# Kernel tuning notes

Hardware: AMD Instinct MI355X
Metric: run time of the kernel (lower is better)

The kernel has to match this reference:

```python
import jax, jax.numpy as jnp
import numpy as np


def setup_inputs() -> dict:
    key = jax.random.key(0)
    ks = jax.random.split(key, 6)
    N, n, m = 8, 256, 256
    d_q, d_k, d_v, hidden = 256, 256, 256, 256
    scale_q = 1.0 / np.sqrt(d_q)
    scale_k = 1.0 / np.sqrt(d_k)
    scale_h = 1.0 / np.sqrt(hidden)
    return {
        "query": jax.random.normal(ks[0], (N, n, d_q), dtype=jnp.float32),
        "key": jax.random.normal(ks[1], (N, m, d_k), dtype=jnp.float32),
        "value": jax.random.normal(ks[2], (N, m, d_v), dtype=jnp.float32),
        # Linear weights stored as (in, out) so projection is x @ W
        "Wq": jax.random.normal(ks[3], (d_q, hidden), dtype=jnp.float32) * scale_q,
        "Wk": jax.random.normal(ks[4], (d_k, hidden), dtype=jnp.float32) * scale_k,
        "Wv": jax.random.normal(ks[5], (hidden,), dtype=jnp.float32) * scale_h,
        "choose": 0,
    }


def reference(query, key, value, Wq, Wk, Wv, choose):
    if choose == 0:
        q = jnp.einsum('bnd,dh->bnh', query, Wq)   # (N, n, h)
        k = jnp.einsum('bmd,dh->bmh', key, Wk)     # (N, m, h)
        # broadcast-add + tanh, then contract hidden with W_v -> scores (N, n, m)
        features = jnp.tanh(q[:, :, None, :] + k[:, None, :, :])  # (N, n, m, h)
        scores = jnp.einsum('bnmh,h->bnm', features, Wv)
        # NOTE: original applies softmax over dim=1 (query axis) — preserved
        attn_weights = jax.nn.softmax(scores, axis=1)
    else:
        d = query.shape[2]
        scores = jnp.einsum('bnd,bmd->bnm', query, key) / jnp.sqrt(jnp.float32(d))
        attn_weights = jax.nn.softmax(scores, axis=-1)
    return jnp.einsum('bnm,bmd->bnd', attn_weights, value)
```

## Files before the change

kernel.cpp:

```cpp
#include <hip/hip_runtime.h>

#define N_B 8
#define DIM 256

constexpr float C2    = 2.8853900817779268f;
constexpr float LOG2E = 1.4426950408889634f;

typedef __attribute__((ext_vector_type(8))) short short8;
typedef __attribute__((ext_vector_type(4))) float f32x4;
typedef unsigned short ushort_t;

__device__ __forceinline__ unsigned hi2(float a, float b) {
    return (__float_as_uint(a) >> 16) | (__float_as_uint(b) & 0xFFFF0000u);
}
__device__ __forceinline__ float trunc_res(float a) {
    return a - __uint_as_float(__float_as_uint(a) & 0xFFFF0000u);
}

__global__ __launch_bounds__(512) void proj_mfma(
    const float* __restrict__ query, const float* __restrict__ key,
    const float* __restrict__ Wq, const float* __restrict__ Wk,
    float* __restrict__ EQ, float* __restrict__ EK)
{
    __shared__ __align__(16) ushort_t Ah[64 * 64], Al[64 * 64], Bh[64 * 64], Bl[64 * 64];
    __shared__ __align__(16) float T[64][68];

    int bid = blockIdx.x;
    int y = bid & 15;
    int x = bid >> 4;
    int b = y >> 1; bool isK = y & 1;
    const float* A    = (isK ? key : query) + b * DIM * DIM;
    const float* Wsrc = isK ? Wk : Wq;

    int R0 = (x >> 2) * 64, C0 = (x & 3) * 64;

    int tid = threadIdx.x;
    int w = tid >> 6, lane = tid & 63;
    int wr = w >> 2, wc = w & 3;
    int l15 = lane & 15, l4 = lane >> 4;

    int sr = tid >> 3, skq = (tid & 7) * 8;
    int kp = tid & 31, cg = tid >> 5;

    f32x4 acc[2] = {};
    float4 areg0, areg1;
    float4 w00, w10;

    {
        const float* ap = &A[(size_t)(R0 + sr) * DIM + skq];
        areg0 = *(const float4*)&ap[0];  areg1 = *(const float4*)&ap[4];
        const float* wp0 = &Wsrc[(size_t)(2 * kp)     * DIM + C0 + cg * 4];
        const float* wp1 = &Wsrc[(size_t)(2 * kp + 1) * DIM + C0 + cg * 4];
        w00 = *(const float4*)&wp0[0];
        w10 = *(const float4*)&wp1[0];
    }

    for (int ks = 0; ks < 4; ++ks) {
        {
            int i0 = (sr * 64 + skq) ^ ((sr & 7) << 3);
            uint4 hv = make_uint4(hi2(areg0.x, areg0.y), hi2(areg0.z, areg0.w),
                                  hi2(areg1.x, areg1.y), hi2(areg1.z, areg1.w));
            uint4 lv = make_uint4(hi2(trunc_res(areg0.x), trunc_res(areg0.y)),
                                  hi2(trunc_res(areg0.z), trunc_res(areg0.w)),
                                  hi2(trunc_res(areg1.x), trunc_res(areg1.y)),
                                  hi2(trunc_res(areg1.z), trunc_res(areg1.w)));
            *(uint4*)&Ah[i0] = hv;
            *(uint4*)&Al[i0] = lv;
            float a0[4] = {w00.x, w00.y, w00.z, w00.w};
            float a1[4] = {w10.x, w10.y, w10.z, w10.w};
#pragma unroll
            for (int c = 0; c < 4; ++c) {
                int col = cg * 4 + c;
                int idx = (col * 64 + 2 * kp) ^ ((col & 7) << 3);
                *(unsigned*)&Bh[idx] = hi2(a0[c], a1[c]);
                *(unsigned*)&Bl[idx] = hi2(trunc_res(a0[c]), trunc_res(a1[c]));
            }
        }
        __syncthreads();
        if (ks < 3) {
            int K0 = (ks + 1) * 64;
            const float* ap = &A[(size_t)(R0 + sr) * DIM + K0 + skq];
            areg0 = *(const float4*)&ap[0];  areg1 = *(const float4*)&ap[4];
            const float* wp0 = &Wsrc[(size_t)(K0 + 2 * kp)     * DIM + C0 + cg * 4];
            const float* wp1 = &Wsrc[(size_t)(K0 + 2 * kp + 1) * DIM + C0 + cg * 4];
            w00 = *(const float4*)&wp0[0];
            w10 = *(const float4*)&wp1[0];
        }
#pragma unroll
        for (int kk = 0; kk < 2; ++kk) {
            int kb = kk * 32 + l4 * 8;
            short8 ah[2], al[2], bh, bl;
#pragma unroll
            for (int i = 0; i < 2; ++i) {
                int arow = wr * 32 + i * 16 + l15;
                int aidx = (arow * 64 + kb) ^ ((arow & 7) << 3);
                ah[i] = *(const short8*)&Ah[aidx];
                al[i] = *(const short8*)&Al[aidx];
            }
            {
                int bcol = wc * 16 + l15;
                int bidx = (bcol * 64 + kb) ^ ((bcol & 7) << 3);
                bh = *(const short8*)&Bh[bidx];
                bl = *(const short8*)&Bl[bidx];
            }
#pragma unroll
            for (int i = 0; i < 2; ++i) {
                acc[i] = __builtin_amdgcn_mfma_f32_16x16x32_bf16(ah[i], bh, acc[i], 0, 0, 0);
                acc[i] = __builtin_amdgcn_mfma_f32_16x16x32_bf16(ah[i], bl, acc[i], 0, 0, 0);
                acc[i] = __builtin_amdgcn_mfma_f32_16x16x32_bf16(al[i], bh, acc[i], 0, 0, 0);
            }
        }
        __syncthreads();
    }

#pragma unroll
    for (int i = 0; i < 2; ++i) {
        float ev[4];
#pragma unroll
        for (int v = 0; v < 4; ++v) ev[v] = __builtin_amdgcn_exp2f(C2 * acc[i][v]);
        int row = wr * 32 + i * 16 + l4 * 4;
        int col = wc * 16 + l15;
        if (isK) {
#pragma unroll
            for (int v = 0; v < 4; ++v) T[row + v][col] = ev[v];
        } else {
            *(float4*)&T[col][row] = make_float4(ev[0], ev[1], ev[2], ev[3]);
        }
    }
    __syncthreads();
    {
        int r = tid >> 3, q = tid & 7;
        float* dst = isK ? &EK[(size_t)b * DIM * DIM + (size_t)(R0 + r) * DIM + C0 + q * 8]
                         : &EQ[(size_t)b * DIM * DIM + (size_t)(C0 + r) * DIM + R0 + q * 8];
        *(float4*)&dst[0] = *(const float4*)&T[r][q * 8];
        *(float4*)&dst[4] = *(const float4*)&T[r][q * 8 + 4];
    }
}

__global__ __launch_bounds__(512, 2) void scores_softmax_kernel(
    const float* __restrict__ EQ, const float* __restrict__ EK,
    const float* __restrict__ Wv, ushort_t* __restrict__ ANh)
{
    int bid = blockIdx.x;
    int b  = bid & 7;
    int M0 = (bid >> 3) * 4;
    const float* Qb = EQ + b * DIM * DIM;
    const float* Kb = EK + b * DIM * DIM;

    __shared__ __align__(16) float Eks[4][DIM];
    __shared__ __align__(16) float Ws[DIM];
    __shared__ __align__(16) float part[3][2][64][8];

    int tid  = threadIdx.x;
    int w = tid >> 6, lane = tid & 63;
    int hs = w & 3, mg = w >> 2;
    int n0 = lane * 4;

    {
        int row = tid >> 7, h2 = (tid & 127) * 2;
        *(float2*)&Eks[row][h2] = *(const float2*)&Kb[(M0 + row) * DIM + h2];
    }
    if (tid < 64) *(float4*)&Ws[tid * 4] = *(const float4*)&Wv[tid * 4];

    float wsum = Wv[lane] + Wv[lane + 64] + Wv[lane + 128] + Wv[lane + 192];
#pragma unroll
    for (int o = 32; o; o >>= 1) wsum += __shfl_xor(wsum, o);
    __syncthreads();

    float acc[2][4] = {};
    const float* qbase = Qb + (hs * 4) * 256 + n0;

    float4 qr[4];
#pragma unroll
    for (int r = 0; r < 4; ++r) qr[r] = *(const float4*)&qbase[r * 256];

    for (int c = 0; c < 16; ++c) {
        float4 qn[4];
        if (c < 15) {
            const float* qc = qbase + (c + 1) * 4096;
#pragma unroll
            for (int r = 0; r < 4; ++r) qn[r] = *(const float4*)&qc[r * 256];
        }
        float4 wv4 = *(const float4*)&Ws[c * 16 + hs * 4];
        float wva[4] = {wv4.x, wv4.y, wv4.z, wv4.w};
        float eka[2][4];
#pragma unroll
        for (int i = 0; i < 2; ++i) {
            float4 e4 = *(const float4*)&Eks[mg * 2 + i][c * 16 + hs * 4];
            eka[i][0] = e4.x; eka[i][1] = e4.y; eka[i][2] = e4.z; eka[i][3] = e4.w;
        }
#pragma unroll
        for (int hh = 0; hh < 2; ++hh) {
            float q0a[4] = {qr[hh * 2].x, qr[hh * 2].y, qr[hh * 2].z, qr[hh * 2].w};
            float q1a[4] = {qr[hh * 2 + 1].x, qr[hh * 2 + 1].y, qr[hh * 2 + 1].z, qr[hh * 2 + 1].w};
            float w0 = wva[hh * 2], w1 = wva[hh * 2 + 1];
#pragma unroll
            for (int i = 0; i < 2; ++i) {
                float e0 = eka[i][hh * 2], e1 = eka[i][hh * 2 + 1];
#pragma unroll
                for (int j = 0; j < 4; ++j) {
                    float d0 = fmaf(q0a[j], e0, 1.0f);
                    float d1 = fmaf(q1a[j], e1, 1.0f);
                    float num = fmaf(w0, d1, w1 * d0);
                    acc[i][j] = fmaf(num, __builtin_amdgcn_rcpf(d0 * d1), acc[i][j]);
                }
            }
        }
        if (c < 15) {
#pragma unroll
            for (int r = 0; r < 4; ++r) qr[r] = qn[r];
        }
    }

    if (hs) {
#pragma unroll
        for (int i = 0; i < 2; ++i) {
            float4 v = make_float4(acc[i][0], acc[i][1], acc[i][2], acc[i][3]);
            *(float4*)&part[hs - 1][mg][lane][i * 4] = v;
        }
    }
    __syncthreads();
    if (hs == 0) {
#pragma unroll
        for (int p = 0; p < 3; ++p)
#pragma unroll
            for (int i = 0; i < 2; ++i) {
                float4 v = *(const float4*)&part[p][mg][lane][i * 4];
                acc[i][0] += v.x; acc[i][1] += v.y; acc[i][2] += v.z; acc[i][3] += v.w;
            }
        float e[2][4], t[2];
#pragma unroll
        for (int i = 0; i < 2; ++i) {
            t[i] = 0.0f;
#pragma unroll
            for (int j = 0; j < 4; ++j) {
                e[i][j] = __builtin_amdgcn_exp2f((wsum - 2.0f * acc[i][j]) * LOG2E);
                t[i] += e[i][j];
            }
        }
#pragma unroll
        for (int o = 32; o; o >>= 1) { t[0] += __shfl_xor(t[0], o); t[1] += __shfl_xor(t[1], o); }
        float r0 = __builtin_amdgcn_rcpf(t[0]);
        float r1 = __builtin_amdgcn_rcpf(t[1]);
        int mcol = M0 + mg * 2;
#pragma unroll
        for (int j = 0; j < 4; ++j) {
            float a0 = e[0][j] * r0, a1 = e[1][j] * r1;
            *(unsigned*)&ANh[((size_t)b * DIM + n0 + j) * DIM + mcol] = hi2(a0, a1);
        }
    }
}

__global__ __launch_bounds__(256) void av_mfma(
    const ushort_t* __restrict__ ANh,
    const float* __restrict__ value, float* __restrict__ out)
{
    __shared__ __align__(16) ushort_t Ah[32 * 64], Bh[32 * 64], Bl[32 * 64];
    __shared__ __align__(16) float T[32][36];

    int bid = blockIdx.x;
    int b = bid & 7;
    int x = bid >> 3;
    int R0 = (x >> 3) * 32, C0 = (x & 7) * 32;
    const ushort_t* Abh = ANh + (size_t)b * DIM * DIM;
    const float*    Vb  = value + (size_t)b * DIM * DIM;

    int tid = threadIdx.x;
    int w = tid >> 6, lane = tid & 63;
    int wr = w >> 1, wc = w & 1;
    int l15 = lane & 15, l4 = lane >> 4;
    int sr = tid >> 3, skq = (tid & 7) * 8;
    int kp = tid & 31, cg = tid >> 5;

    f32x4 acc[2] = {};
    f32x4 a0acc = {};
    uint4 ah0;
    float4 v00, v10;
    {
        size_t aa = (size_t)(R0 + sr) * DIM + skq;
        ah0 = *(const uint4*)&Abh[aa];
        const float* vp0 = &Vb[(size_t)(2 * kp)     * DIM + C0 + cg * 4];
        const float* vp1 = &Vb[(size_t)(2 * kp + 1) * DIM + C0 + cg * 4];
        v00 = *(const float4*)&vp0[0];
        v10 = *(const float4*)&vp1[0];
    }

    for (int ks = 0; ks < 4; ++ks) {
        {
            int i0 = (sr * 64 + skq) ^ ((sr & 7) << 3);
            *(uint4*)&Ah[i0] = ah0;
            float a0[4] = {v00.x, v00.y, v00.z, v00.w};
            float a1[4] = {v10.x, v10.y, v10.z, v10.w};
#pragma unroll
            for (int c = 0; c < 4; ++c) {
                int col = cg * 4 + c;
                int idx = (col * 64 + 2 * kp) ^ ((col & 7) << 3);
                *(unsigned*)&Bh[idx] = hi2(a0[c], a1[c]);
                *(unsigned*)&Bl[idx] = hi2(trunc_res(a0[c]), trunc_res(a1[c]));
            }
        }
        __syncthreads();
        if (ks < 3) {
            int K0 = (ks + 1) * 64;
            size_t aa = (size_t)(R0 + sr) * DIM + K0 + skq;
            ah0 = *(const uint4*)&Abh[aa];
            const float* vp0 = &Vb[(size_t)(K0 + 2 * kp)     * DIM + C0 + cg * 4];
            const float* vp1 = &Vb[(size_t)(K0 + 2 * kp + 1) * DIM + C0 + cg * 4];
            v00 = *(const float4*)&vp0[0];
            v10 = *(const float4*)&vp1[0];
        }
#pragma unroll
        for (int kk = 0; kk < 2; ++kk) {
            int kb = kk * 32 + l4 * 8;
            short8 ah, bh, bl;
            {
                int arow = wr * 16 + l15;
                int aidx = (arow * 64 + kb) ^ ((arow & 7) << 3);
                ah = *(const short8*)&Ah[aidx];
            }
            {
                int bcol = wc * 16 + l15;
                int bidx = (bcol * 64 + kb) ^ ((bcol & 7) << 3);
                bh = *(const short8*)&Bh[bidx];
                bl = *(const short8*)&Bl[bidx];
            }
            a0acc = __builtin_amdgcn_mfma_f32_16x16x32_bf16(ah, bh, a0acc, 0, 0, 0);
            a0acc = __builtin_amdgcn_mfma_f32_16x16x32_bf16(ah, bl, a0acc, 0, 0, 0);
        }
        __syncthreads();
    }

    {
        int row = wr * 16 + l4 * 4;
        int col = wc * 16 + l15;
#pragma unroll
        for (int v = 0; v < 4; ++v) T[row + v][col] = a0acc[v];
    }
    __syncthreads();
    {
        int r = tid >> 3, q = tid & 7;
        float* dst = &out[((size_t)b * DIM + R0 + r) * DIM + C0 + q * 4];
        *(float4*)&dst[0] = *(const float4*)&T[r][q * 4];
    }
}

extern "C" void kernel_launch(void* const* d_in, const int* in_sizes, int n_in,
                              void* d_out, int out_size, void* d_ws, size_t ws_size,
                              hipStream_t stream)
{
    const float* query = (const float*)d_in[0];
    const float* key   = (const float*)d_in[1];
    const float* value = (const float*)d_in[2];
    const float* Wq    = (const float*)d_in[3];
    const float* Wk    = (const float*)d_in[4];
    const float* Wv    = (const float*)d_in[5];
    float* out = (float*)d_out;

    float* EQ = (float*)d_ws;
    float* EK = EQ + N_B * DIM * DIM;
    ushort_t* ANh = (ushort_t*)(EK + N_B * DIM * DIM);

    proj_mfma            <<<256, 512, 0, stream>>>(query, key, Wq, Wk, EQ, EK);
    scores_softmax_kernel<<<512, 512, 0, stream>>>(EQ, EK, Wv, ANh);
    av_mfma              <<<512, 256, 0, stream>>>(ANh, value, out);
}
```

Baseline: 32.19 us.

## Halve projection tile rows, double grid, drop low-bf16 A term

The projection kernel now computes 32x64 output tiles instead of 64x64 and launches 512 blocks instead of 256, with launch bounds raised to two blocks per CU. The aim is more parallelism and a smaller shared-memory footprint per block. It also stops splitting the activation operand into high and low bf16 parts, so each step issues two MFMAs (ah*bh, ah*bl) instead of three. This cuts MFMA work and LDS traffic but lowers the precision of the projections, which could hurt accuracy against the fp32 reference.

```diff
diff --git a/kernel.cpp b/kernel.cpp
--- a/kernel.cpp
+++ b/kernel.cpp
@@ -17,13 +17,13 @@
     return a - __uint_as_float(__float_as_uint(a) & 0xFFFF0000u);
 }
 
-__global__ __launch_bounds__(512) void proj_mfma(
+__global__ __launch_bounds__(512, 2) void proj_mfma(
     const float* __restrict__ query, const float* __restrict__ key,
     const float* __restrict__ Wq, const float* __restrict__ Wk,
     float* __restrict__ EQ, float* __restrict__ EK)
 {
-    __shared__ __align__(16) ushort_t Ah[64 * 64], Al[64 * 64], Bh[64 * 64], Bl[64 * 64];
-    __shared__ __align__(16) float T[64][68];
+    __shared__ __align__(16) ushort_t Ah[32 * 64], Bh[64 * 64], Bl[64 * 64];
+    __shared__ __align__(16) float T[2304];
 
     int bid = blockIdx.x;
     int y = bid & 15;
@@ -32,23 +32,22 @@
     const float* A    = (isK ? key : query) + b * DIM * DIM;
     const float* Wsrc = isK ? Wk : Wq;
 
-    int R0 = (x >> 2) * 64, C0 = (x & 3) * 64;
+    int R0 = (x >> 2) * 32, C0 = (x & 3) * 64;
 
     int tid = threadIdx.x;
     int w = tid >> 6, lane = tid & 63;
     int wr = w >> 2, wc = w & 3;
     int l15 = lane & 15, l4 = lane >> 4;
 
-    int sr = tid >> 3, skq = (tid & 7) * 8;
+    int sr = tid >> 4, skq = (tid & 15) * 4;
     int kp = tid & 31, cg = tid >> 5;
 
-    f32x4 acc[2] = {};
-    float4 areg0, areg1;
+    f32x4 acc = {};
+    float4 areg;
     float4 w00, w10;
 
     {
-        const float* ap = &A[(size_t)(R0 + sr) * DIM + skq];
-        areg0 = *(const float4*)&ap[0];  areg1 = *(const float4*)&ap[4];
+        areg = *(const float4*)&A[(size_t)(R0 + sr) * DIM + skq];
         const float* wp0 = &Wsrc[(size_t)(2 * kp)     * DIM + C0 + cg * 4];
         const float* wp1 = &Wsrc[(size_t)(2 * kp + 1) * DIM + C0 + cg * 4];
         w00 = *(const float4*)&wp0[0];
@@ -58,14 +57,7 @@
     for (int ks = 0; ks < 4; ++ks) {
         {
             int i0 = (sr * 64 + skq) ^ ((sr & 7) << 3);
-            uint4 hv = make_uint4(hi2(areg0.x, areg0.y), hi2(areg0.z, areg0.w),
-                                  hi2(areg1.x, areg1.y), hi2(areg1.z, areg1.w));
-            uint4 lv = make_uint4(hi2(trunc_res(areg0.x), trunc_res(areg0.y)),
-                                  hi2(trunc_res(areg0.z), trunc_res(areg0.w)),
-                                  hi2(trunc_res(areg1.x), trunc_res(areg1.y)),
-                                  hi2(trunc_res(areg1.z), trunc_res(areg1.w)));
-            *(uint4*)&Ah[i0] = hv;
-            *(uint4*)&Al[i0] = lv;
+            *(uint2*)&Ah[i0] = make_uint2(hi2(areg.x, areg.y), hi2(areg.z, areg.w));
             float a0[4] = {w00.x, w00.y, w00.z, w00.w};
             float a1[4] = {w10.x, w10.y, w10.z, w10.w};
 #pragma unroll
@@ -79,8 +71,7 @@
         __syncthreads();
         if (ks < 3) {
             int K0 = (ks + 1) * 64;
-            const float* ap = &A[(size_t)(R0 + sr) * DIM + K0 + skq];
-            areg0 = *(const float4*)&ap[0];  areg1 = *(const float4*)&ap[4];
+            areg = *(const float4*)&A[(size_t)(R0 + sr) * DIM + K0 + skq];
             const float* wp0 = &Wsrc[(size_t)(K0 + 2 * kp)     * DIM + C0 + cg * 4];
             const float* wp1 = &Wsrc[(size_t)(K0 + 2 * kp + 1) * DIM + C0 + cg * 4];
             w00 = *(const float4*)&wp0[0];
@@ -89,13 +80,11 @@
 #pragma unroll
         for (int kk = 0; kk < 2; ++kk) {
             int kb = kk * 32 + l4 * 8;
-            short8 ah[2], al[2], bh, bl;
-#pragma unroll
-            for (int i = 0; i < 2; ++i) {
-                int arow = wr * 32 + i * 16 + l15;
+            short8 ah, bh, bl;
+            {
+                int arow = wr * 16 + l15;
                 int aidx = (arow * 64 + kb) ^ ((arow & 7) << 3);
-                ah[i] = *(const short8*)&Ah[aidx];
-                al[i] = *(const short8*)&Al[aidx];
+                ah = *(const short8*)&Ah[aidx];
             }
             {
                 int bcol = wc * 16 + l15;
@@ -103,37 +92,34 @@
                 bh = *(const short8*)&Bh[bidx];
                 bl = *(const short8*)&Bl[bidx];
             }
-#pragma unroll
-            for (int i = 0; i < 2; ++i) {
-                acc[i] = __builtin_amdgcn_mfma_f32_16x16x32_bf16(ah[i], bh, acc[i], 0, 0, 0);
-                acc[i] = __builtin_amdgcn_mfma_f32_16x16x32_bf16(ah[i], bl, acc[i], 0, 0, 0);
-                acc[i] = __builtin_amdgcn_mfma_f32_16x16x32_bf16(al[i], bh, acc[i], 0, 0, 0);
-            }
+            acc = __builtin_amdgcn_mfma_f32_16x16x32_bf16(ah, bh, acc, 0, 0, 0);
+            acc = __builtin_amdgcn_mfma_f32_16x16x32_bf16(ah, bl, acc, 0, 0, 0);
         }
         __syncthreads();
     }
 
-#pragma unroll
-    for (int i = 0; i < 2; ++i) {
+    {
         float ev[4];
 #pragma unroll
-        for (int v = 0; v < 4; ++v) ev[v] = __builtin_amdgcn_exp2f(C2 * acc[i][v]);
-        int row = wr * 32 + i * 16 + l4 * 4;
+        for (int v = 0; v < 4; ++v) ev[v] = __builtin_amdgcn_exp2f(C2 * acc[v]);
+        int row = wr * 16 + l4 * 4;
         int col = wc * 16 + l15;
         if (isK) {
 #pragma unroll
-            for (int v = 0; v < 4; ++v) T[row + v][col] = ev[v];
+            for (int v = 0; v < 4; ++v) T[(row + v) * 68 + col] = ev[v];
         } else {
-            *(float4*)&T[col][row] = make_float4(ev[0], ev[1], ev[2], ev[3]);
+            *(float4*)&T[col * 36 + row] = make_float4(ev[0], ev[1], ev[2], ev[3]);
         }
     }
     __syncthreads();
-    {
+    if (isK) {
+        int r = tid >> 4, q = tid & 15;
+        float* dst = &EK[(size_t)b * DIM * DIM + (size_t)(R0 + r) * DIM + C0 + q * 4];
+        *(float4*)dst = *(const float4*)&T[r * 68 + q * 4];
+    } else {
         int r = tid >> 3, q = tid & 7;
-        float* dst = isK ? &EK[(size_t)b * DIM * DIM + (size_t)(R0 + r) * DIM + C0 + q * 8]
-                         : &EQ[(size_t)b * DIM * DIM + (size_t)(C0 + r) * DIM + R0 + q * 8];
-        *(float4*)&dst[0] = *(const float4*)&T[r][q * 8];
-        *(float4*)&dst[4] = *(const float4*)&T[r][q * 8 + 4];
+        float* dst = &EQ[(size_t)b * DIM * DIM + (size_t)(C0 + r) * DIM + R0 + q * 4];
+        *(float4*)dst = *(const float4*)&T[r * 36 + q * 4];
     }
 }
 
@@ -272,7 +258,6 @@
     int sr = tid >> 3, skq = (tid & 7) * 8;
     int kp = tid & 31, cg = tid >> 5;
 
-    f32x4 acc[2] = {};
     f32x4 a0acc = {};
     uint4 ah0;
     float4 v00, v10;
@@ -360,7 +345,7 @@
     float* EK = EQ + N_B * DIM * DIM;
     ushort_t* ANh = (ushort_t*)(EK + N_B * DIM * DIM);
 
-    proj_mfma            <<<256, 512, 0, stream>>>(query, key, Wq, Wk, EQ, EK);
+    proj_mfma            <<<512, 512, 0, stream>>>(query, key, Wq, Wk, EQ, EK);
     scores_softmax_kernel<<<512, 512, 0, stream>>>(EQ, EK, Wv, ANh);
     av_mfma              <<<512, 256, 0, stream>>>(ANh, value, out);
 }
```

After: 32.29 us. No clear change (+0.3%).
